# Kernel tuning notes

Hardware: AMD Instinct MI355X
Metric: run time of the kernel (lower is better)

## Reference

```python
import jax, jax.numpy as jnp
import numpy as np

N_EXPERTS = 8
TOP_K = 2


def setup_inputs() -> dict:
    key = jax.random.key(0)
    ks = jax.random.split(key, 5)
    B, T, D, E, H = 4, 2048, 1024, N_EXPERTS, 2730  # H = int(2*D*4/3)
    x = jax.random.normal(ks[0], (B, T, D), dtype=jnp.float32)
    gate_w = jax.random.normal(ks[1], (E, D), dtype=jnp.float32) * 0.02
    w1 = jax.random.normal(ks[2], (E, H, D), dtype=jnp.float32) * 0.02
    w3 = jax.random.normal(ks[3], (E, H, D), dtype=jnp.float32) * 0.02
    w2 = jax.random.normal(ks[4], (E, D, H), dtype=jnp.float32) * 0.02
    return {"x": x, "gate_w": gate_w, "w1": w1, "w3": w3, "w2": w2}


def reference(x, gate_w, w1, w3, w2):
    B, T, D = x.shape
    E = gate_w.shape[0]
    x_flat = x.reshape(-1, D)  # [N, D], N = B*T
    N = x_flat.shape[0]

    # Router: top-k over softmax probabilities, renormalized over selected experts
    logits = x_flat @ gate_w.T                      # [N, E]
    probs = jax.nn.softmax(logits, axis=-1)         # [N, E]
    top_v, top_i = jax.lax.top_k(probs, TOP_K)      # [N, K]
    top_v = top_v / jnp.sum(top_v, axis=-1, keepdims=True)

    # Dense combine weights [N, E]: weight of expert e for each token (0 if not selected).
    # top_k indices are distinct per token, so scatter-add equals scatter-set here.
    combine = jnp.zeros((N, E), dtype=x.dtype).at[
        jnp.arange(N)[:, None], top_i
    ].add(top_v)

    # Weighted combine of SwiGLU experts (loop over small fixed expert count).
    out = jnp.zeros_like(x_flat)
    for e in range(E):
        gate = jax.nn.silu(x_flat @ w1[e].T)        # [N, H]
        up = x_flat @ w3[e].T                       # [N, H]
        y = (gate * up) @ w2[e].T                   # [N, D]
        out = out + combine[:, e:e + 1] * y

    aux_loss = jnp.asarray(0.0, dtype=x.dtype)  # use_aux_loss=False / eval mode
    return out.reshape(B, T, D), aux_loss
```

## Files before the change

### kernel.cpp

```cpp
#include <hip/hip_runtime.h>
#include <hip/hip_bf16.h>

#define N_TOK 8192
#define D_DIM 1024
#define E_NUM 8
#define H_DIM 2730
#define HP    2816
#define HP8   (HP/8)
#define NROWS (N_TOK*2)
#define MAXTILES 136

typedef __bf16 bf16;
typedef __bf16 bf16x8 __attribute__((ext_vector_type(8)));
typedef __bf16 bf16x4 __attribute__((ext_vector_type(4)));
typedef float  f32x4  __attribute__((ext_vector_type(4)));

__device__ __forceinline__ void gload_lds16(const bf16* g, bf16* l) {
  __builtin_amdgcn_global_load_lds((const __attribute__((address_space(1))) void*)g,
                                   (__attribute__((address_space(3))) void*)l, 16, 0, 0);
}

#define VMCNT(n) asm volatile("s_waitcnt vmcnt(" #n ")" ::: "memory")

__global__ void conv13_kernel(const float* __restrict__ s1, const float* __restrict__ s3,
                              bf16* __restrict__ d1, bf16* __restrict__ d3, int n8) {
  int i = blockIdx.x * blockDim.x + threadIdx.x;
  if (i >= n8) return;
  const float4* p1 = (const float4*)s1 + i * 2;
  const float4* p3 = (const float4*)s3 + i * 2;
  float4 a0 = p1[0], a1 = p1[1], b0 = p3[0], b1 = p3[1];
  bf16x8 o1, o3;
  o1[0]=(bf16)a0.x; o1[1]=(bf16)a0.y; o1[2]=(bf16)a0.z; o1[3]=(bf16)a0.w;
  o1[4]=(bf16)a1.x; o1[5]=(bf16)a1.y; o1[6]=(bf16)a1.z; o1[7]=(bf16)a1.w;
  o3[0]=(bf16)b0.x; o3[1]=(bf16)b0.y; o3[2]=(bf16)b0.z; o3[3]=(bf16)b0.w;
  o3[4]=(bf16)b1.x; o3[5]=(bf16)b1.y; o3[6]=(bf16)b1.z; o3[7]=(bf16)b1.w;
  ((bf16x8*)d1)[i] = o1;
  ((bf16x8*)d3)[i] = o3;
}

__global__ void conv_w2_kernel(const float* __restrict__ src, bf16* __restrict__ dst) {
  int i = blockIdx.x * blockDim.x + threadIdx.x;
  if (i >= E_NUM * D_DIM * HP8) return;
  int c8 = i % HP8;
  int row = i / HP8;
  int c = c8 * 8;
  const float* s = src + (long)row * H_DIM + c;
  bf16x8 o;
  #pragma unroll
  for (int j = 0; j < 8; j++) o[j] = (c + j < H_DIM) ? (bf16)s[j] : (bf16)0.f;
  ((bf16x8*)dst)[i] = o;
}

__global__ void router_kernel(const float* __restrict__ x, const float* __restrict__ gw,
                              int* __restrict__ topi, float* __restrict__ topw,
                              int* __restrict__ counts) {
  int t = blockIdx.x * (blockDim.x >> 6) + (threadIdx.x >> 6);
  int lane = threadIdx.x & 63;
  if (t >= N_TOK) return;
  const float* xr = x + (long)t * D_DIM;
  float acc[E_NUM];
  #pragma unroll
  for (int e = 0; e < E_NUM; e++) acc[e] = 0.f;
  for (int j = 0; j < D_DIM / 64; j++) {
    float xv = xr[j * 64 + lane];
    #pragma unroll
    for (int e = 0; e < E_NUM; e++) acc[e] += xv * gw[e * D_DIM + j * 64 + lane];
  }
  #pragma unroll
  for (int e = 0; e < E_NUM; e++) {
    float v = acc[e];
    #pragma unroll
    for (int s = 32; s > 0; s >>= 1) v += __shfl_xor(v, s, 64);
    acc[e] = v;
  }
  if (lane == 0) {
    int b0 = -1, b1 = -1; float v0 = -1e30f, v1 = -1e30f;
    #pragma unroll
    for (int e = 0; e < E_NUM; e++) {
      float v = acc[e];
      if (v > v0) { v1 = v0; b1 = b0; v0 = v; b0 = e; }
      else if (v > v1) { v1 = v; b1 = e; }
    }
    float w0 = 1.f / (1.f + expf(v1 - v0));
    topi[t * 2] = b0; topi[t * 2 + 1] = b1;
    topw[t * 2] = w0; topw[t * 2 + 1] = 1.f - w0;
    atomicAdd(&counts[b0], 1); atomicAdd(&counts[b1], 1);
  }
}

__global__ void tiles_kernel(const int* __restrict__ counts, int* __restrict__ offs,
                             int* __restrict__ tlist) {
  if (threadIdx.x == 0) {
    int s = 0, idx = 0;
    for (int e = 0; e < E_NUM; e++) {
      offs[e] = s;
      int ne = counts[e];
      s += ne;
      int nt = (ne + 127) >> 7;
      for (int t = 0; t < nt; t++) tlist[idx++] = (e << 8) | t;
    }
    offs[E_NUM] = s;
    for (; idx < MAXTILES; idx++) tlist[idx] = -1;
  }
}

__global__ void scatter_kernel(const int* __restrict__ topi, const float* __restrict__ topw,
                               const int* __restrict__ offs, int* __restrict__ cursor,
                               int* __restrict__ rowmap, float* __restrict__ roww,
                               int* __restrict__ rowoftok) {
  int i = blockIdx.x * blockDim.x + threadIdx.x;
  if (i >= NROWS) return;
  int e = topi[i];
  int pos = atomicAdd(&cursor[e], 1);
  int row = offs[e] + pos;
  rowmap[row] = i >> 1;
  roww[row] = topw[i];
  rowoftok[i] = row;
}

__global__ void gather_kernel(const float* __restrict__ x, const int* __restrict__ rowmap,
                              bf16* __restrict__ Xg) {
  int r = blockIdx.x * (blockDim.x >> 6) + (threadIdx.x >> 6);
  int lane = threadIdx.x & 63;
  if (r >= NROWS) return;
  int t = rowmap[r];
  const float4* src = (const float4*)(x + (long)t * D_DIM);
  bf16x4* dst = (bf16x4*)(Xg + (long)r * D_DIM);
  #pragma unroll
  for (int j = 0; j < 4; j++) {
    float4 v = src[j * 64 + lane];
    bf16x4 o; o[0]=(bf16)v.x; o[1]=(bf16)v.y; o[2]=(bf16)v.z; o[3]=(bf16)v.w;
    dst[j * 64 + lane] = o;
  }
}

__global__ void combine_kernel(const bf16* __restrict__ y, const int* __restrict__ rowoftok,
                               const float* __restrict__ topw, float* __restrict__ out) {
  int t = blockIdx.x * (blockDim.x >> 6) + (threadIdx.x >> 6);
  int lane = threadIdx.x & 63;
  if (t >= N_TOK) return;
  int r0 = rowoftok[t * 2], r1 = rowoftok[t * 2 + 1];
  float w0 = topw[t * 2], w1 = topw[t * 2 + 1];
  const bf16x8* y0 = (const bf16x8*)(y + (long)r0 * D_DIM);
  const bf16x8* y1 = (const bf16x8*)(y + (long)r1 * D_DIM);
  float* o = out + (long)t * D_DIM;
  #pragma unroll
  for (int j = 0; j < 2; j++) {
    bf16x8 a = y0[j * 64 + lane], b = y1[j * 64 + lane];
    float4 v0, v1;
    v0.x = w0*(float)a[0] + w1*(float)b[0]; v0.y = w0*(float)a[1] + w1*(float)b[1];
    v0.z = w0*(float)a[2] + w1*(float)b[2]; v0.w = w0*(float)a[3] + w1*(float)b[3];
    v1.x = w0*(float)a[4] + w1*(float)b[4]; v1.y = w0*(float)a[5] + w1*(float)b[5];
    v1.z = w0*(float)a[6] + w1*(float)b[6]; v1.w = w0*(float)a[7] + w1*(float)b[7];
    float4* op = (float4*)(o + (j * 64 + lane) * 8);
    op[0] = v0; op[1] = v1;
  }
}


#define G1_STAGE(OFF, K0) do { \
    _Pragma("unroll") \
    for (int i_ = 0; i_ < 2; i_++) { \
      gload_lds16(aptr[i_] + (K0), &smem1[(OFF) + (i_ * 4 + w) * 512]); \
      gload_lds16(b1ptr[i_] + (K0), &smem1[(OFF) + 4096 + (i_ * 4 + w) * 512]); \
      gload_lds16(b3ptr[i_] + (K0), &smem1[(OFF) + 8192 + (i_ * 4 + w) * 512]); \
    } } while (0)

#define G1_COMPUTE(OFF) do { \
    bf16x8 af[4], b1f[4], b3f[4]; \
    _Pragma("unroll") \
    for (int m_ = 0; m_ < 4; m_++) af[m_] = *(const bf16x8*)&smem1[(OFF) + (wr * 64 + m_ * 16 + fr) * 32 + qp]; \
    _Pragma("unroll") \
    for (int n_ = 0; n_ < 4; n_++) { \
      b1f[n_] = *(const bf16x8*)&smem1[(OFF) + 4096 + (wc * 64 + n_ * 16 + fr) * 32 + qp]; \
      b3f[n_] = *(const bf16x8*)&smem1[(OFF) + 8192 + (wc * 64 + n_ * 16 + fr) * 32 + qp]; } \
    _Pragma("unroll") \
    for (int m_ = 0; m_ < 4; m_++) \
      _Pragma("unroll") \
      for (int n_ = 0; n_ < 4; n_++) { \
        acc1[m_][n_] = __builtin_amdgcn_mfma_f32_16x16x32_bf16(af[m_], b1f[n_], acc1[m_][n_], 0, 0, 0); \
        acc3[m_][n_] = __builtin_amdgcn_mfma_f32_16x16x32_bf16(af[m_], b3f[n_], acc3[m_][n_], 0, 0, 0); \
      } } while (0)

__global__ __launch_bounds__(256, 2) void gemm1_kernel(
    const bf16* __restrict__ Xg, const bf16* __restrict__ w1b, const bf16* __restrict__ w3b,
    const int* __restrict__ counts, const int* __restrict__ offs,
    const int* __restrict__ tlist, bf16* __restrict__ h) {
  int te = tlist[blockIdx.x];
  if (te < 0) return;
  int e = te >> 8, tm = te & 255;
  int ne = counts[e];
  int row_base = offs[e];
  int n0 = blockIdx.y * 128;

  __shared__ bf16 smem1[3 * 12288];
  int tid = threadIdx.x, w = tid >> 6, lane = tid & 63;
  int wr = w >> 1, wc = w & 1;
  int seg_r = lane >> 2;
  int seg_c = (((lane & 3) ^ ((lane >> 3) & 3))) * 8;
  int fr = lane & 15;
  int qp = (((lane >> 4) ^ ((fr >> 1) & 3))) * 8;

  f32x4 acc1[4][4], acc3[4][4];
  #pragma unroll
  for (int m = 0; m < 4; m++)
    #pragma unroll
    for (int n = 0; n < 4; n++) { acc1[m][n] = (f32x4)0.f; acc3[m][n] = (f32x4)0.f; }

  const bf16* w1e = w1b + (long)e * H_DIM * D_DIM;
  const bf16* w3e = w3b + (long)e * H_DIM * D_DIM;

  const bf16* aptr[2];
  const bf16* b1ptr[2];
  const bf16* b3ptr[2];
  #pragma unroll
  for (int i = 0; i < 2; i++) {
    int ra = row_base + min(tm * 128 + (i * 4 + w) * 16 + seg_r, ne - 1);
    aptr[i] = Xg + (long)ra * D_DIM + seg_c;
    int rb = min(n0 + (i * 4 + w) * 16 + seg_r, H_DIM - 1);
    b1ptr[i] = w1e + (long)rb * D_DIM + seg_c;
    b3ptr[i] = w3e + (long)rb * D_DIM + seg_c;
  }

  int o0 = 0, o1 = 12288, o2 = 24576;
  G1_STAGE(o0, 0);
  G1_STAGE(o1, 32);
  #define G1_ROT() do { int t_ = o0; o0 = o1; o1 = o2; o2 = t_; } while (0)
  for (int t = 0; t < D_DIM / 32 - 2; t++) {
    G1_STAGE(o2, (t + 2) * 32);
    VMCNT(12);
    __builtin_amdgcn_s_barrier();
    G1_COMPUTE(o0);
    __builtin_amdgcn_s_barrier();
    G1_ROT();
  }
  VMCNT(6);
  __builtin_amdgcn_s_barrier();
  G1_COMPUTE(o0);
  __builtin_amdgcn_s_barrier();
  G1_ROT();
  VMCNT(0);
  __builtin_amdgcn_s_barrier();
  G1_COMPUTE(o0);

  int crow4 = (lane >> 4) * 4, ccol = lane & 15;
  #pragma unroll
  for (int m = 0; m < 4; m++)
    #pragma unroll
    for (int j = 0; j < 4; j++) {
      int rloc = tm * 128 + wr * 64 + m * 16 + crow4 + j;
      if (rloc < ne) {
        long hrow = (long)(row_base + rloc) * HP;
        #pragma unroll
        for (int n = 0; n < 4; n++) {
          int col = n0 + wc * 64 + n * 16 + ccol;
          float g = acc1[m][n][j], u = acc3[m][n][j];
          float hv = (col < H_DIM) ? (g / (1.f + __expf(-g))) * u : 0.f;
          h[hrow + col] = (bf16)hv;
        }
      }
    }
}

#define G2_STAGE(OFF, K0) do { \
    _Pragma("unroll") \
    for (int i_ = 0; i_ < 2; i_++) { \
      gload_lds16(aptr[i_] + (K0), &smem2[(OFF) + (i_ * 4 + w) * 512]); \
      gload_lds16(bptr[i_] + (K0), &smem2[(OFF) + 4096 + (i_ * 4 + w) * 512]); \
    } } while (0)

#define G2_COMPUTE(OFF) do { \
    bf16x8 af[4], bfr[4]; \
    _Pragma("unroll") \
    for (int m_ = 0; m_ < 4; m_++) af[m_] = *(const bf16x8*)&smem2[(OFF) + (wr * 64 + m_ * 16 + fr) * 32 + qp]; \
    _Pragma("unroll") \
    for (int n_ = 0; n_ < 4; n_++) bfr[n_] = *(const bf16x8*)&smem2[(OFF) + 4096 + (wc * 64 + n_ * 16 + fr) * 32 + qp]; \
    _Pragma("unroll") \
    for (int m_ = 0; m_ < 4; m_++) \
      _Pragma("unroll") \
      for (int n_ = 0; n_ < 4; n_++) \
        acc[m_][n_] = __builtin_amdgcn_mfma_f32_16x16x32_bf16(af[m_], bfr[n_], acc[m_][n_], 0, 0, 0); \
    } while (0)

__global__ __launch_bounds__(256, 2) void gemm2_kernel(
    const bf16* __restrict__ h, const bf16* __restrict__ w2b,
    const int* __restrict__ counts, const int* __restrict__ offs,
    const int* __restrict__ tlist, bf16* __restrict__ y) {
  int te = tlist[blockIdx.x];
  if (te < 0) return;
  int e = te >> 8, tm = te & 255;
  int ne = counts[e];
  int row_base = offs[e];
  int n0 = blockIdx.y * 128;

  __shared__ bf16 smem2[3 * 8192];
  int tid = threadIdx.x, w = tid >> 6, lane = tid & 63;
  int wr = w >> 1, wc = w & 1;
  int seg_r = lane >> 2;
  int seg_c = (((lane & 3) ^ ((lane >> 3) & 3))) * 8;
  int fr = lane & 15;
  int qp = (((lane >> 4) ^ ((fr >> 1) & 3))) * 8;

  f32x4 acc[4][4];
  #pragma unroll
  for (int m = 0; m < 4; m++)
    #pragma unroll
    for (int n = 0; n < 4; n++) acc[m][n] = (f32x4)0.f;

  const bf16* w2e = w2b + (long)e * D_DIM * HP;

  const bf16* aptr[2];
  const bf16* bptr[2];
  #pragma unroll
  for (int i = 0; i < 2; i++) {
    int ra = row_base + min(tm * 128 + (i * 4 + w) * 16 + seg_r, ne - 1);
    aptr[i] = h + (long)ra * HP + seg_c;
    bptr[i] = w2e + (long)(n0 + (i * 4 + w) * 16 + seg_r) * HP + seg_c;
  }

  int o0 = 0, o1 = 8192, o2 = 16384;
  G2_STAGE(o0, 0);
  G2_STAGE(o1, 32);
  #define G2_ROT() do { int t_ = o0; o0 = o1; o1 = o2; o2 = t_; } while (0)
  for (int t = 0; t < HP / 32 - 2; t++) {
    G2_STAGE(o2, (t + 2) * 32);
    VMCNT(8);
    __builtin_amdgcn_s_barrier();
    G2_COMPUTE(o0);
    __builtin_amdgcn_s_barrier();
    G2_ROT();
  }
  VMCNT(4);
  __builtin_amdgcn_s_barrier();
  G2_COMPUTE(o0);
  __builtin_amdgcn_s_barrier();
  G2_ROT();
  VMCNT(0);
  __builtin_amdgcn_s_barrier();
  G2_COMPUTE(o0);

  int crow4 = (lane >> 4) * 4, ccol = lane & 15;
  #pragma unroll
  for (int m = 0; m < 4; m++)
    #pragma unroll
    for (int j = 0; j < 4; j++) {
      int rloc = tm * 128 + wr * 64 + m * 16 + crow4 + j;
      if (rloc < ne) {
        long yrow = (long)(row_base + rloc) * D_DIM;
        #pragma unroll
        for (int n = 0; n < 4; n++) {
          int col = n0 + wc * 64 + n * 16 + ccol;
          y[yrow + col] = (bf16)acc[m][n][j];
        }
      }
    }
}

extern "C" void kernel_launch(void* const* d_in, const int* in_sizes, int n_in,
                              void* d_out, int out_size, void* d_ws, size_t ws_size,
                              hipStream_t stream) {
  const float* x  = (const float*)d_in[0];
  const float* gw = (const float*)d_in[1];
  const float* w1 = (const float*)d_in[2];
  const float* w3 = (const float*)d_in[3];
  const float* w2 = (const float*)d_in[4];
  float* out = (float*)d_out;

  char* ws = (char*)d_ws;
  int*   counts   = (int*)(ws);
  int*   cursor   = (int*)(ws + 64);
  int*   offs     = (int*)(ws + 128);
  int*   tlist    = (int*)(ws + 192);
  int*   topi     = (int*)(ws + 1024);
  float* topw     = (float*)(ws + 1024 + 65536);
  int*   rowmap   = (int*)(ws + 1024 + 131072);
  float* roww     = (float*)(ws + 1024 + 196608);
  int*   rowoftok = (int*)(ws + 1024 + 262144);
  char*  big      = ws + 1024 + 327680;
  bf16* w1b = (bf16*)big;
  bf16* w3b = w1b + (size_t)E_NUM * H_DIM * D_DIM;
  bf16* w2b = w3b + (size_t)E_NUM * H_DIM * D_DIM;
  bf16* Xg  = w2b + (size_t)E_NUM * D_DIM * HP;
  bf16* hbuf = Xg + (size_t)NROWS * D_DIM;
  bf16* ybuf = Xg;

  hipMemsetAsync((char*)d_out + (size_t)(out_size - 1) * sizeof(float), 0, sizeof(float), stream);
  hipMemsetAsync(ws, 0, 256, stream);

  int n8 = E_NUM * H_DIM * D_DIM / 8;
  conv13_kernel<<<(n8 + 255) / 256, 256, 0, stream>>>(w1, w3, w1b, w3b, n8);
  int w2n = E_NUM * D_DIM * HP8;
  conv_w2_kernel<<<(w2n + 255) / 256, 256, 0, stream>>>(w2, w2b);

  router_kernel<<<N_TOK / 4, 256, 0, stream>>>(x, gw, topi, topw, counts);
  tiles_kernel<<<1, 64, 0, stream>>>(counts, offs, tlist);
  scatter_kernel<<<(NROWS + 255) / 256, 256, 0, stream>>>(topi, topw, offs, cursor, rowmap, roww, rowoftok);
  gather_kernel<<<NROWS / 4, 256, 0, stream>>>(x, rowmap, Xg);

  dim3 g1(MAXTILES, 22);
  gemm1_kernel<<<g1, 256, 0, stream>>>(Xg, w1b, w3b, counts, offs, tlist, hbuf);
  dim3 g2(MAXTILES, 8);
  gemm2_kernel<<<g2, 256, 0, stream>>>(hbuf, w2b, counts, offs, tlist, ybuf);
  combine_kernel<<<N_TOK / 4, 256, 0, stream>>>(ybuf, rowoftok, topw, out);
}
```

Before: 767.5 us.

## Interleave w1/w3 weights and enlarge GEMM tiles for expert FFN

Converts w1 and w3 into one interleaved bf16 matrix, 16 rows of each alternating, so gemm1 treats gate and up as a single 256-wide N tile. gemm1 moves to 256x256 tiles with 512 threads, a double-buffered pipeline and MFMA priority boosting. gemm2 widens its N tile to 256. The w2 conversion now runs after gemm1 so its buffer can share workspace with the interleaved weights. Larger tiles raise data reuse and cut redundant weight loads, but add register pressure and more padding waste on ragged per-expert tiles.

```diff
diff --git a/kernel.cpp b/kernel.cpp
--- a/kernel.cpp
+++ b/kernel.cpp
@@ -6,9 +6,10 @@
 #define E_NUM 8
 #define H_DIM 2730
 #define HP    2816
-#define HP8   (HP/8)
+#define NP    5632
 #define NROWS (N_TOK*2)
 #define MAXTILES 136
+#define MAXT256  72
 
 typedef __bf16 bf16;
 typedef __bf16 bf16x8 __attribute__((ext_vector_type(8)));
@@ -19,30 +20,35 @@
   __builtin_amdgcn_global_load_lds((const __attribute__((address_space(1))) void*)g,
                                    (__attribute__((address_space(3))) void*)l, 16, 0, 0);
 }
-
 #define VMCNT(n) asm volatile("s_waitcnt vmcnt(" #n ")" ::: "memory")
-
-__global__ void conv13_kernel(const float* __restrict__ s1, const float* __restrict__ s3,
-                              bf16* __restrict__ d1, bf16* __restrict__ d3, int n8) {
+#define BAR() __builtin_amdgcn_s_barrier()
+
+__global__ void conv13_kernel(const float* __restrict__ w1, const float* __restrict__ w3,
+                              bf16* __restrict__ Bp) {
   int i = blockIdx.x * blockDim.x + threadIdx.x;
-  if (i >= n8) return;
-  const float4* p1 = (const float4*)s1 + i * 2;
-  const float4* p3 = (const float4*)s3 + i * 2;
-  float4 a0 = p1[0], a1 = p1[1], b0 = p3[0], b1 = p3[1];
-  bf16x8 o1, o3;
-  o1[0]=(bf16)a0.x; o1[1]=(bf16)a0.y; o1[2]=(bf16)a0.z; o1[3]=(bf16)a0.w;
-  o1[4]=(bf16)a1.x; o1[5]=(bf16)a1.y; o1[6]=(bf16)a1.z; o1[7]=(bf16)a1.w;
-  o3[0]=(bf16)b0.x; o3[1]=(bf16)b0.y; o3[2]=(bf16)b0.z; o3[3]=(bf16)b0.w;
-  o3[4]=(bf16)b1.x; o3[5]=(bf16)b1.y; o3[6]=(bf16)b1.z; o3[7]=(bf16)b1.w;
-  ((bf16x8*)d1)[i] = o1;
-  ((bf16x8*)d3)[i] = o3;
+  if (i >= E_NUM * NP * 128) return;
+  int c8 = i & 127;
+  int r  = (i >> 7) % NP;
+  int e  = i / (NP * 128);
+  int hc = ((r >> 5) << 4) + (r & 15);
+  bf16x8 o;
+  if (hc < H_DIM) {
+    const float* s = (((r >> 4) & 1) ? w3 : w1) + ((long)e * H_DIM + hc) * D_DIM + c8 * 8;
+    float4 a0 = ((const float4*)s)[0], a1 = ((const float4*)s)[1];
+    o[0]=(bf16)a0.x; o[1]=(bf16)a0.y; o[2]=(bf16)a0.z; o[3]=(bf16)a0.w;
+    o[4]=(bf16)a1.x; o[5]=(bf16)a1.y; o[6]=(bf16)a1.z; o[7]=(bf16)a1.w;
+  } else {
+    #pragma unroll
+    for (int j = 0; j < 8; j++) o[j] = (bf16)0.f;
+  }
+  ((bf16x8*)Bp)[i] = o;
 }
 
 __global__ void conv_w2_kernel(const float* __restrict__ src, bf16* __restrict__ dst) {
   int i = blockIdx.x * blockDim.x + threadIdx.x;
-  if (i >= E_NUM * D_DIM * HP8) return;
-  int c8 = i % HP8;
-  int row = i / HP8;
+  if (i >= E_NUM * D_DIM * (HP / 8)) return;
+  int c8 = i % (HP / 8);
+  int row = i / (HP / 8);
   int c = c8 * 8;
   const float* s = src + (long)row * H_DIM + c;
   bf16x8 o;
@@ -89,18 +95,21 @@
 }
 
 __global__ void tiles_kernel(const int* __restrict__ counts, int* __restrict__ offs,
-                             int* __restrict__ tlist) {
+                             int* __restrict__ tlist, int* __restrict__ tlist2) {
   if (threadIdx.x == 0) {
-    int s = 0, idx = 0;
+    int s = 0, idx = 0, idx2 = 0;
     for (int e = 0; e < E_NUM; e++) {
       offs[e] = s;
       int ne = counts[e];
       s += ne;
       int nt = (ne + 127) >> 7;
       for (int t = 0; t < nt; t++) tlist[idx++] = (e << 8) | t;
+      int nt2 = (ne + 255) >> 8;
+      for (int t = 0; t < nt2; t++) tlist2[idx2++] = (e << 8) | t;
     }
     offs[E_NUM] = s;
     for (; idx < MAXTILES; idx++) tlist[idx] = -1;
+    for (; idx2 < MAXT256; idx2++) tlist2[idx2] = -1;
   }
 }
 
@@ -157,130 +166,143 @@
   }
 }
 
-
-#define G1_STAGE(OFF, K0) do { \
-    _Pragma("unroll") \
-    for (int i_ = 0; i_ < 2; i_++) { \
-      gload_lds16(aptr[i_] + (K0), &smem1[(OFF) + (i_ * 4 + w) * 512]); \
-      gload_lds16(b1ptr[i_] + (K0), &smem1[(OFF) + 4096 + (i_ * 4 + w) * 512]); \
-      gload_lds16(b3ptr[i_] + (K0), &smem1[(OFF) + 8192 + (i_ * 4 + w) * 512]); \
-    } } while (0)
-
-#define G1_COMPUTE(OFF) do { \
-    bf16x8 af[4], b1f[4], b3f[4]; \
-    _Pragma("unroll") \
-    for (int m_ = 0; m_ < 4; m_++) af[m_] = *(const bf16x8*)&smem1[(OFF) + (wr * 64 + m_ * 16 + fr) * 32 + qp]; \
-    _Pragma("unroll") \
-    for (int n_ = 0; n_ < 4; n_++) { \
-      b1f[n_] = *(const bf16x8*)&smem1[(OFF) + 4096 + (wc * 64 + n_ * 16 + fr) * 32 + qp]; \
-      b3f[n_] = *(const bf16x8*)&smem1[(OFF) + 8192 + (wc * 64 + n_ * 16 + fr) * 32 + qp]; } \
-    _Pragma("unroll") \
-    for (int m_ = 0; m_ < 4; m_++) \
-      _Pragma("unroll") \
-      for (int n_ = 0; n_ < 4; n_++) { \
-        acc1[m_][n_] = __builtin_amdgcn_mfma_f32_16x16x32_bf16(af[m_], b1f[n_], acc1[m_][n_], 0, 0, 0); \
-        acc3[m_][n_] = __builtin_amdgcn_mfma_f32_16x16x32_bf16(af[m_], b3f[n_], acc3[m_][n_], 0, 0, 0); \
-      } } while (0)
-
-__global__ __launch_bounds__(256, 2) void gemm1_kernel(
-    const bf16* __restrict__ Xg, const bf16* __restrict__ w1b, const bf16* __restrict__ w3b,
+#define G1_READ_A(MH, OB) do { \
+    _Pragma("unroll") for (int m_ = 0; m_ < 4; m_++) \
+    _Pragma("unroll") for (int ks_ = 0; ks_ < 2; ks_++) \
+      aF[m_][ks_] = *(const bf16x8*)&smem[(OB) + ((MH)*128 + wr*64 + m_*16 + fr)*64 + ((ks_*4 + hi) ^ fr7)*8]; \
+  } while (0)
+#define G1_READ_B(NH, OB) do { \
+    _Pragma("unroll") for (int n_ = 0; n_ < 2; n_++) \
+    _Pragma("unroll") for (int ks_ = 0; ks_ < 2; ks_++) \
+      bF[n_][ks_] = *(const bf16x8*)&smem[(OB) + 16384 + ((NH)*128 + wc*32 + n_*16 + fr)*64 + ((ks_*4 + hi) ^ fr7)*8]; \
+  } while (0)
+#define G1_MFMA(MH, NH) do { \
+    __builtin_amdgcn_s_setprio(1); \
+    _Pragma("unroll") for (int m_ = 0; m_ < 4; m_++) \
+    _Pragma("unroll") for (int n_ = 0; n_ < 2; n_++) \
+    _Pragma("unroll") for (int ks_ = 0; ks_ < 2; ks_++) \
+      acc[MH][NH][m_][n_] = __builtin_amdgcn_mfma_f32_16x16x32_bf16(aF[m_][ks_], bF[n_][ks_], acc[MH][NH][m_][n_], 0, 0, 0); \
+    __builtin_amdgcn_s_setprio(0); \
+  } while (0)
+#define G1_STAGE_A(NB, HM, KT) do { \
+    _Pragma("unroll") for (int L_ = 0; L_ < 2; L_++) \
+      gload_lds16(aP[HM][L_] + (KT)*64, smem + (NB)*32768 + ((HM)*128 + wv*16 + L_*8)*64); \
+  } while (0)
+#define G1_STAGE_B(NB, HM, KT) do { \
+    _Pragma("unroll") for (int L_ = 0; L_ < 2; L_++) \
+      gload_lds16(bP[HM][L_] + (KT)*64, smem + (NB)*32768 + 16384 + ((HM)*128 + wv*16 + L_*8)*64); \
+  } while (0)
+
+__global__ __launch_bounds__(512, 2) void gemm1_kernel(
+    const bf16* __restrict__ Xg, const bf16* __restrict__ Bp,
     const int* __restrict__ counts, const int* __restrict__ offs,
-    const int* __restrict__ tlist, bf16* __restrict__ h) {
-  int te = tlist[blockIdx.x];
+    const int* __restrict__ tlist2, bf16* __restrict__ h) {
+  int te = tlist2[blockIdx.x];
   if (te < 0) return;
   int e = te >> 8, tm = te & 255;
   int ne = counts[e];
   int row_base = offs[e];
-  int n0 = blockIdx.y * 128;
-
-  __shared__ bf16 smem1[3 * 12288];
-  int tid = threadIdx.x, w = tid >> 6, lane = tid & 63;
-  int wr = w >> 1, wc = w & 1;
-  int seg_r = lane >> 2;
-  int seg_c = (((lane & 3) ^ ((lane >> 3) & 3))) * 8;
-  int fr = lane & 15;
-  int qp = (((lane >> 4) ^ ((fr >> 1) & 3))) * 8;
-
-  f32x4 acc1[4][4], acc3[4][4];
-  #pragma unroll
-  for (int m = 0; m < 4; m++)
-    #pragma unroll
-    for (int n = 0; n < 4; n++) { acc1[m][n] = (f32x4)0.f; acc3[m][n] = (f32x4)0.f; }
-
-  const bf16* w1e = w1b + (long)e * H_DIM * D_DIM;
-  const bf16* w3e = w3b + (long)e * H_DIM * D_DIM;
-
-  const bf16* aptr[2];
-  const bf16* b1ptr[2];
-  const bf16* b3ptr[2];
-  #pragma unroll
-  for (int i = 0; i < 2; i++) {
-    int ra = row_base + min(tm * 128 + (i * 4 + w) * 16 + seg_r, ne - 1);
-    aptr[i] = Xg + (long)ra * D_DIM + seg_c;
-    int rb = min(n0 + (i * 4 + w) * 16 + seg_r, H_DIM - 1);
-    b1ptr[i] = w1e + (long)rb * D_DIM + seg_c;
-    b3ptr[i] = w3e + (long)rb * D_DIM + seg_c;
-  }
-
-  int o0 = 0, o1 = 12288, o2 = 24576;
-  G1_STAGE(o0, 0);
-  G1_STAGE(o1, 32);
-  #define G1_ROT() do { int t_ = o0; o0 = o1; o1 = o2; o2 = t_; } while (0)
-  for (int t = 0; t < D_DIM / 32 - 2; t++) {
-    G1_STAGE(o2, (t + 2) * 32);
-    VMCNT(12);
-    __builtin_amdgcn_s_barrier();
-    G1_COMPUTE(o0);
-    __builtin_amdgcn_s_barrier();
-    G1_ROT();
-  }
-  VMCNT(6);
-  __builtin_amdgcn_s_barrier();
-  G1_COMPUTE(o0);
-  __builtin_amdgcn_s_barrier();
-  G1_ROT();
-  VMCNT(0);
-  __builtin_amdgcn_s_barrier();
-  G1_COMPUTE(o0);
-
-  int crow4 = (lane >> 4) * 4, ccol = lane & 15;
-  #pragma unroll
-  for (int m = 0; m < 4; m++)
-    #pragma unroll
-    for (int j = 0; j < 4; j++) {
-      int rloc = tm * 128 + wr * 64 + m * 16 + crow4 + j;
-      if (rloc < ne) {
-        long hrow = (long)(row_base + rloc) * HP;
+  int n0 = blockIdx.y * 256;
+
+  __shared__ bf16 smem[2 * 32768];
+  int tid = threadIdx.x, wv = tid >> 6, lane = tid & 63;
+  int wr = wv >> 2, wc = wv & 3;
+  int fr = lane & 15, hi = lane >> 4, fr7 = lane & 7;
+  int l8 = lane >> 3;
+  int sx = ((lane & 7) ^ (l8 & 7)) * 8;
+
+  f32x4 acc[2][2][4][2];
+  #pragma unroll
+  for (int a = 0; a < 2; a++)
+    #pragma unroll
+    for (int b = 0; b < 2; b++)
+      #pragma unroll
+      for (int m = 0; m < 4; m++)
         #pragma unroll
-        for (int n = 0; n < 4; n++) {
-          int col = n0 + wc * 64 + n * 16 + ccol;
-          float g = acc1[m][n][j], u = acc3[m][n][j];
-          float hv = (col < H_DIM) ? (g / (1.f + __expf(-g))) * u : 0.f;
-          h[hrow + col] = (bf16)hv;
+        for (int n = 0; n < 2; n++) acc[a][b][m][n] = (f32x4)0.f;
+
+  const bf16* Bpe = Bp + (long)e * NP * D_DIM;
+  const bf16* aP[2][2];
+  const bf16* bP[2][2];
+  #pragma unroll
+  for (int hm = 0; hm < 2; hm++)
+    #pragma unroll
+    for (int L = 0; L < 2; L++) {
+      int rt = tm * 256 + hm * 128 + wv * 16 + L * 8 + l8;
+      aP[hm][L] = Xg + (long)(row_base + min(rt, ne - 1)) * D_DIM + sx;
+      int rb = n0 + hm * 128 + wv * 16 + L * 8 + l8;
+      bP[hm][L] = Bpe + (long)rb * D_DIM + sx;
+    }
+
+  bf16x8 aF[4][2], bF[2][2];
+
+  G1_STAGE_B(0, 0, 0); G1_STAGE_A(0, 0, 0); G1_STAGE_A(0, 1, 0); G1_STAGE_B(0, 1, 0);
+  VMCNT(4); BAR();
+
+  for (int t = 0; t < 15; t++) {
+    int ob = (t & 1) << 15;
+    int nb = (t + 1) & 1;
+    G1_READ_A(0, ob); G1_READ_B(0, ob);
+    G1_STAGE_B(nb, 0, t + 1);
+    VMCNT(4); BAR(); G1_MFMA(0, 0); BAR();
+    G1_READ_A(1, ob);
+    G1_STAGE_A(nb, 0, t + 1);
+    VMCNT(4); BAR(); G1_MFMA(1, 0); BAR();
+    G1_READ_B(1, ob);
+    G1_STAGE_A(nb, 1, t + 1);
+    BAR(); G1_MFMA(1, 1); BAR();
+    G1_READ_A(0, ob);
+    G1_STAGE_B(nb, 1, t + 1);
+    VMCNT(4); BAR(); G1_MFMA(0, 1); BAR();
+  }
+  {
+    const int ob = 32768;
+    G1_READ_A(0, ob); G1_READ_B(0, ob);
+    VMCNT(2); BAR(); G1_MFMA(0, 0); BAR();
+    G1_READ_A(1, ob);
+    VMCNT(0); BAR(); G1_MFMA(1, 0); BAR();
+    G1_READ_B(1, ob);
+    BAR(); G1_MFMA(1, 1); BAR();
+    G1_READ_A(0, ob);
+    G1_MFMA(0, 1);
+  }
+
+  int crow4 = hi * 4, ccol = fr;
+  #pragma unroll
+  for (int mh = 0; mh < 2; mh++)
+    #pragma unroll
+    for (int m = 0; m < 4; m++)
+      #pragma unroll
+      for (int j = 0; j < 4; j++) {
+        int rloc = tm * 256 + mh * 128 + wr * 64 + m * 16 + crow4 + j;
+        if (rloc < ne) {
+          long hrow = (long)(row_base + rloc) * HP;
+          #pragma unroll
+          for (int nh = 0; nh < 2; nh++) {
+            int hc0 = (n0 + nh * 128 + wc * 32) >> 1;
+            float g = acc[mh][nh][m][0][j], u = acc[mh][nh][m][1][j];
+            h[hrow + hc0 + ccol] = (bf16)((g / (1.f + __expf(-g))) * u);
+          }
         }
       }
-    }
 }
 
 #define G2_STAGE(OFF, K0) do { \
-    _Pragma("unroll") \
-    for (int i_ = 0; i_ < 2; i_++) { \
+    _Pragma("unroll") for (int i_ = 0; i_ < 2; i_++) \
       gload_lds16(aptr[i_] + (K0), &smem2[(OFF) + (i_ * 4 + w) * 512]); \
-      gload_lds16(bptr[i_] + (K0), &smem2[(OFF) + 4096 + (i_ * 4 + w) * 512]); \
-    } } while (0)
-
+    _Pragma("unroll") for (int j_ = 0; j_ < 4; j_++) \
+      gload_lds16(bptr[j_] + (K0), &smem2[(OFF) + 4096 + (j_ * 4 + w) * 512]); \
+  } while (0)
 #define G2_COMPUTE(OFF) do { \
-    bf16x8 af[4], bfr[4]; \
-    _Pragma("unroll") \
-    for (int m_ = 0; m_ < 4; m_++) af[m_] = *(const bf16x8*)&smem2[(OFF) + (wr * 64 + m_ * 16 + fr) * 32 + qp]; \
-    _Pragma("unroll") \
-    for (int n_ = 0; n_ < 4; n_++) bfr[n_] = *(const bf16x8*)&smem2[(OFF) + 4096 + (wc * 64 + n_ * 16 + fr) * 32 + qp]; \
-    _Pragma("unroll") \
-    for (int m_ = 0; m_ < 4; m_++) \
-      _Pragma("unroll") \
-      for (int n_ = 0; n_ < 4; n_++) \
-        acc[m_][n_] = __builtin_amdgcn_mfma_f32_16x16x32_bf16(af[m_], bfr[n_], acc[m_][n_], 0, 0, 0); \
-    } while (0)
+    bf16x8 af[4], bfr[8]; \
+    _Pragma("unroll") for (int m_ = 0; m_ < 4; m_++) af[m_] = *(const bf16x8*)&smem2[(OFF) + (wr * 64 + m_ * 16 + fr) * 32 + qp]; \
+    _Pragma("unroll") for (int n_ = 0; n_ < 8; n_++) bfr[n_] = *(const bf16x8*)&smem2[(OFF) + 4096 + (wc * 128 + n_ * 16 + fr) * 32 + qp]; \
+    __builtin_amdgcn_s_setprio(1); \
+    _Pragma("unroll") for (int m_ = 0; m_ < 4; m_++) \
+    _Pragma("unroll") for (int n_ = 0; n_ < 8; n_++) \
+      acc[m_][n_] = __builtin_amdgcn_mfma_f32_16x16x32_bf16(af[m_], bfr[n_], acc[m_][n_], 0, 0, 0); \
+    __builtin_amdgcn_s_setprio(0); \
+  } while (0)
 
 __global__ __launch_bounds__(256, 2) void gemm2_kernel(
     const bf16* __restrict__ h, const bf16* __restrict__ w2b,
@@ -291,53 +313,49 @@
   int e = te >> 8, tm = te & 255;
   int ne = counts[e];
   int row_base = offs[e];
-  int n0 = blockIdx.y * 128;
-
-  __shared__ bf16 smem2[3 * 8192];
+  int n0 = blockIdx.y * 256;
+
+  __shared__ bf16 smem2[3 * 12288];
   int tid = threadIdx.x, w = tid >> 6, lane = tid & 63;
   int wr = w >> 1, wc = w & 1;
-  int seg_r = lane >> 2;
   int seg_c = (((lane & 3) ^ ((lane >> 3) & 3))) * 8;
   int fr = lane & 15;
   int qp = (((lane >> 4) ^ ((fr >> 1) & 3))) * 8;
 
-  f32x4 acc[4][4];
+  f32x4 acc[4][8];
   #pragma unroll
   for (int m = 0; m < 4; m++)
     #pragma unroll
-    for (int n = 0; n < 4; n++) acc[m][n] = (f32x4)0.f;
+    for (int n = 0; n < 8; n++) acc[m][n] = (f32x4)0.f;
 
   const bf16* w2e = w2b + (long)e * D_DIM * HP;
-
   const bf16* aptr[2];
-  const bf16* bptr[2];
+  const bf16* bptr[4];
   #pragma unroll
   for (int i = 0; i < 2; i++) {
-    int ra = row_base + min(tm * 128 + (i * 4 + w) * 16 + seg_r, ne - 1);
+    int ra = row_base + min(tm * 128 + (i * 4 + w) * 16 + (lane >> 2), ne - 1);
     aptr[i] = h + (long)ra * HP + seg_c;
-    bptr[i] = w2e + (long)(n0 + (i * 4 + w) * 16 + seg_r) * HP + seg_c;
-  }
-
-  int o0 = 0, o1 = 8192, o2 = 16384;
+  }
+  #pragma unroll
+  for (int j = 0; j < 4; j++) {
+    int rb = n0 + (j * 4 + w) * 16 + (lane >> 2);
+    bptr[j] = w2e + (long)rb * HP + seg_c;
+  }
+
+  int o0 = 0, o1 = 12288, o2 = 24576;
   G2_STAGE(o0, 0);
   G2_STAGE(o1, 32);
   #define G2_ROT() do { int t_ = o0; o0 = o1; o1 = o2; o2 = t_; } while (0)
   for (int t = 0; t < HP / 32 - 2; t++) {
     G2_STAGE(o2, (t + 2) * 32);
-    VMCNT(8);
-    __builtin_amdgcn_s_barrier();
+    VMCNT(12);
+    BAR();
     G2_COMPUTE(o0);
-    __builtin_amdgcn_s_barrier();
+    BAR();
     G2_ROT();
   }
-  VMCNT(4);
-  __builtin_amdgcn_s_barrier();
-  G2_COMPUTE(o0);
-  __builtin_amdgcn_s_barrier();
-  G2_ROT();
-  VMCNT(0);
-  __builtin_amdgcn_s_barrier();
-  G2_COMPUTE(o0);
+  VMCNT(6); BAR(); G2_COMPUTE(o0); BAR(); G2_ROT();
+  VMCNT(0); BAR(); G2_COMPUTE(o0);
 
   int crow4 = (lane >> 4) * 4, ccol = lane & 15;
   #pragma unroll
@@ -348,8 +366,8 @@
       if (rloc < ne) {
         long yrow = (long)(row_base + rloc) * D_DIM;
         #pragma unroll
-        for (int n = 0; n < 4; n++) {
-          int col = n0 + wc * 64 + n * 16 + ccol;
+        for (int n = 0; n < 8; n++) {
+          int col = n0 + wc * 128 + n * 16 + ccol;
           y[yrow + col] = (bf16)acc[m][n][j];
         }
       }
@@ -371,35 +389,37 @@
   int*   cursor   = (int*)(ws + 64);
   int*   offs     = (int*)(ws + 128);
   int*   tlist    = (int*)(ws + 192);
-  int*   topi     = (int*)(ws + 1024);
-  float* topw     = (float*)(ws + 1024 + 65536);
-  int*   rowmap   = (int*)(ws + 1024 + 131072);
-  float* roww     = (float*)(ws + 1024 + 196608);
-  int*   rowoftok = (int*)(ws + 1024 + 262144);
-  char*  big      = ws + 1024 + 327680;
-  bf16* w1b = (bf16*)big;
-  bf16* w3b = w1b + (size_t)E_NUM * H_DIM * D_DIM;
-  bf16* w2b = w3b + (size_t)E_NUM * H_DIM * D_DIM;
-  bf16* Xg  = w2b + (size_t)E_NUM * D_DIM * HP;
+  int*   tlist2   = (int*)(ws + 768);
+  int*   topi     = (int*)(ws + 2048);
+  float* topw     = (float*)(ws + 2048 + 65536);
+  int*   rowmap   = (int*)(ws + 2048 + 131072);
+  float* roww     = (float*)(ws + 2048 + 196608);
+  int*   rowoftok = (int*)(ws + 2048 + 262144);
+  char*  big      = ws + 2048 + 327680;
+  bf16* Bp   = (bf16*)big;
+  bf16* w2b  = (bf16*)big;
+  bf16* Xg   = Bp + (size_t)E_NUM * NP * D_DIM;
   bf16* hbuf = Xg + (size_t)NROWS * D_DIM;
   bf16* ybuf = Xg;
 
   hipMemsetAsync((char*)d_out + (size_t)(out_size - 1) * sizeof(float), 0, sizeof(float), stream);
   hipMemsetAsync(ws, 0, 256, stream);
 
-  int n8 = E_NUM * H_DIM * D_DIM / 8;
-  conv13_kernel<<<(n8 + 255) / 256, 256, 0, stream>>>(w1, w3, w1b, w3b, n8);
-  int w2n = E_NUM * D_DIM * HP8;
-  conv_w2_kernel<<<(w2n + 255) / 256, 256, 0, stream>>>(w2, w2b);
+  int nbp = E_NUM * NP * 128;
+  conv13_kernel<<<(nbp + 255) / 256, 256, 0, stream>>>(w1, w3, Bp);
 
   router_kernel<<<N_TOK / 4, 256, 0, stream>>>(x, gw, topi, topw, counts);
-  tiles_kernel<<<1, 64, 0, stream>>>(counts, offs, tlist);
+  tiles_kernel<<<1, 64, 0, stream>>>(counts, offs, tlist, tlist2);
   scatter_kernel<<<(NROWS + 255) / 256, 256, 0, stream>>>(topi, topw, offs, cursor, rowmap, roww, rowoftok);
   gather_kernel<<<NROWS / 4, 256, 0, stream>>>(x, rowmap, Xg);
 
-  dim3 g1(MAXTILES, 22);
-  gemm1_kernel<<<g1, 256, 0, stream>>>(Xg, w1b, w3b, counts, offs, tlist, hbuf);
-  dim3 g2(MAXTILES, 8);
+  dim3 g1(MAXT256, NP / 256);
+  gemm1_kernel<<<g1, 512, 0, stream>>>(Xg, Bp, counts, offs, tlist2, hbuf);
+
+  int w2n = E_NUM * D_DIM * (HP / 8);
+  conv_w2_kernel<<<(w2n + 255) / 256, 256, 0, stream>>>(w2, w2b);
+
+  dim3 g2(MAXTILES, 4);
   gemm2_kernel<<<g2, 256, 0, stream>>>(hbuf, w2b, counts, offs, tlist, ybuf);
   combine_kernel<<<N_TOK / 4, 256, 0, stream>>>(ybuf, rowoftok, topw, out);
 }
```

Result: no change. 752.6 us (-1.9%).
